# Performance work log

Hardware: AMD Instinct MI355X
Metric: run time of the kernel (lower is better)

## Reference

```python
import jax, jax.numpy as jnp
import numpy as np

B, T, C = 2, 2048, 1024
N_HEAD = 16
HEAD_DIM = C // N_HEAD


def setup_inputs() -> dict:
    key = jax.random.key(0)
    k1, k2, k3 = jax.random.split(key, 3)
    x = jax.random.normal(k1, (B, T, C), dtype=jnp.float32)
    w_attn = jax.random.normal(k2, (C, 3 * C), dtype=jnp.float32) * 0.02
    b_attn = jnp.zeros((3 * C,), dtype=jnp.float32)
    w_proj = jax.random.normal(k3, (C, C), dtype=jnp.float32) * 0.02
    b_proj = jnp.zeros((C,), dtype=jnp.float32)
    return {"x": x, "w_attn": w_attn, "b_attn": b_attn, "w_proj": w_proj, "b_proj": b_proj}


def reference(x, w_attn, b_attn, w_proj, b_proj):
    Bz, Tz, Cz = x.shape
    qkv = x @ w_attn + b_attn                       # [B, T, 3C]
    q, k, v = jnp.split(qkv, 3, axis=-1)
    # [B, H, T, D]
    q = q.reshape(Bz, Tz, N_HEAD, HEAD_DIM).transpose(0, 2, 1, 3)
    k = k.reshape(Bz, Tz, N_HEAD, HEAD_DIM).transpose(0, 2, 1, 3)
    v = v.reshape(Bz, Tz, N_HEAD, HEAD_DIM).transpose(0, 2, 1, 3)
    scale = 1.0 / np.sqrt(HEAD_DIM).astype(np.float32)
    att = jnp.einsum('bhqd,bhkd->bhqk', q, k) * scale  # [B, H, T, T]
    causal = jnp.tril(jnp.ones((Tz, Tz), dtype=bool))
    att = jnp.where(causal[None, None], att, -jnp.inf)
    att = jax.nn.softmax(att, axis=-1)
    y = jnp.einsum('bhqk,bhkd->bhqd', att, v)          # [B, H, T, D]
    y = y.transpose(0, 2, 1, 3).reshape(Bz, Tz, Cz)
    return y @ w_proj + b_proj
```

## Files before the change

### kernel.cpp

```cpp
#include <hip/hip_runtime.h>
#include <stdint.h>

#define T_SEQ 2048
#define NH 16
#define HD 64
#define M_DIM 4096
#define K_DIM 1024

typedef __attribute__((ext_vector_type(8))) short bf16x8;
typedef __attribute__((ext_vector_type(4))) short bf16x4;
typedef __attribute__((ext_vector_type(4))) float f32x4;
typedef __attribute__((ext_vector_type(4))) unsigned short u16x4;

__device__ __forceinline__ unsigned short f2bf(float f) {
  union { float f; uint32_t u; } x; x.f = f;
  uint32_t u = x.u;
  return (unsigned short)((u + 0x7fffu + ((u >> 16) & 1u)) >> 16);
}

__device__ __forceinline__ uint32_t cvtpk_bf16(float a, float b) {
  uint32_t r;
  asm("v_cvt_pk_bf16_f32 %0, %1, %2" : "=v"(r) : "v"(a), "v"(b));
  return r;
}

__device__ __forceinline__ f32x4 mfma16(bf16x4 a, bf16x4 b, f32x4 c) {
  asm("v_mfma_f32_16x16x16_bf16 %0, %1, %2, %0" : "+v"(c) : "v"(a), "v"(b));
  return c;
}

#define GLOAD16(g, l) __builtin_amdgcn_global_load_lds( \
    (const __attribute__((address_space(1))) unsigned int*)(g), \
    (__attribute__((address_space(3))) unsigned int*)(l), 16, 0, 0)

__device__ __forceinline__ void do_convert(const float* __restrict__ src,
                                           unsigned short* __restrict__ dst, int bid) {
  int idx = (bid * 256 + threadIdx.x) * 4;
  f32x4 v = *(const f32x4*)(src + idx);
  u16x4 o;
  #pragma unroll
  for (int i = 0; i < 4; ++i) o[i] = f2bf(v[i]);
  *(u16x4*)(dst + idx) = o;
}

__device__ __forceinline__ void do_transpose(const float* __restrict__ src,
                                             unsigned short* __restrict__ dst,
                                             int R, int Cn, int bx, int by,
                                             float (*tile)[65]) {
  const int r0 = by * 64, c0 = bx * 64;
  const int t = threadIdx.x;
  const int rr = t >> 4;
  const int c4 = (t & 15) * 4;
  #pragma unroll
  for (int p = 0; p < 4; ++p) {
    f32x4 v = *(const f32x4*)(src + (size_t)(r0 + p * 16 + rr) * Cn + c0 + c4);
    #pragma unroll
    for (int i = 0; i < 4; ++i) tile[p * 16 + rr][c4 + i] = v[i];
  }
  __syncthreads();
  #pragma unroll
  for (int p = 0; p < 4; ++p) {
    const int cl = p * 16 + rr;
    u16x4 o;
    #pragma unroll
    for (int i = 0; i < 4; ++i) o[i] = f2bf(tile[c4 + i][cl]);
    *(u16x4*)(dst + (size_t)(c0 + cl) * R + r0 + c4) = o;
  }
}

__global__ __launch_bounds__(256) void prep_kernel(
    const float* __restrict__ x, unsigned short* __restrict__ xb,
    const float* __restrict__ w_attn, unsigned short* __restrict__ wqkvT,
    const float* __restrict__ w_proj, unsigned short* __restrict__ wprojT) {
  __shared__ float tile[64][65];
  const int b = blockIdx.x;
  if (b < 4096) {
    do_convert(x, xb, b);
  } else if (b < 4096 + 768) {
    const int bid = b - 4096;
    do_transpose(w_attn, wqkvT, 1024, 3072, bid % 48, bid / 48, tile);
  } else {
    const int bid = b - 4864;
    do_transpose(w_proj, wprojT, 1024, 1024, bid % 16, bid / 16, tile);
  }
}

template <int MODE, int WM>
__global__ __launch_bounds__(WM * 128) void gemm2_kernel(
    const unsigned short* __restrict__ A,
    const unsigned short* __restrict__ Bt,
    const float* __restrict__ bias,
    unsigned short* __restrict__ qout,
    unsigned short* __restrict__ kout,
    unsigned short* __restrict__ vTout,
    float* __restrict__ fout) {
  constexpr int BM = WM * 64;
  constexpr int NT = WM * 128;
  constexpr int U_A = BM * 4;
  constexpr int NU = (U_A + 512) / NT;
  __shared__ __align__(16) unsigned short As[2][BM * 32];
  __shared__ __align__(16) unsigned short Bs[2][128 * 32];
  const int t = threadIdx.x;
  const int w = t >> 6, l = t & 63;
  const int wr = w >> 1, wc = w & 1;
  const int lr = l & 15, lg = l >> 4;
  const int br = blockIdx.y, bc = blockIdx.x;

  f32x4 acc[4][4];
  const f32x4 zf = {0.f, 0.f, 0.f, 0.f};
  #pragma unroll
  for (int i = 0; i < 4; ++i)
    #pragma unroll
    for (int j = 0; j < 4; ++j) acc[i][j] = zf;

  const unsigned short* Abase = A + (size_t)(br * BM) * K_DIM;
  const unsigned short* Bbase = Bt + (size_t)(bc * 128) * K_DIM;

  #define STAGE(k0, buf) do {                                                    \
    _Pragma("unroll")                                                            \
    for (int i = 0; i < NU; ++i) {                                               \
      const int u = i * NT + t;                                                  \
      if (u < U_A) {                                                             \
        GLOAD16(Abase + (size_t)(u >> 2) * K_DIM + (k0) + (u & 3) * 8,           \
                &As[buf][u * 8]);                                                \
      } else {                                                                   \
        const int v = u - U_A;                                                   \
        GLOAD16(Bbase + (size_t)(v >> 2) * K_DIM + (k0) + (v & 3) * 8,           \
                &Bs[buf][v * 8]);                                                \
      }                                                                          \
    }                                                                            \
  } while (0)

  #define COMPUTE(buf) do {                                                      \
    bf16x8 af[4], bfv[4];                                                        \
    _Pragma("unroll")                                                            \
    for (int f = 0; f < 4; ++f) {                                                \
      af[f]  = *(const bf16x8*)(&As[buf][(wr * 64 + f * 16 + lr) * 32 + lg * 8]);\
      bfv[f] = *(const bf16x8*)(&Bs[buf][(wc * 64 + f * 16 + lr) * 32 + lg * 8]);\
    }                                                                            \
    _Pragma("unroll")                                                            \
    for (int fr = 0; fr < 4; ++fr)                                               \
      _Pragma("unroll")                                                          \
      for (int fc = 0; fc < 4; ++fc)                                             \
        acc[fr][fc] = __builtin_amdgcn_mfma_f32_16x16x32_bf16(af[fr], bfv[fc],   \
                                                              acc[fr][fc], 0, 0, 0); \
  } while (0)

  STAGE(0, 0);
  __syncthreads();
  #pragma unroll 1
  for (int k0 = 0; k0 < K_DIM; k0 += 64) {
    if (k0 + 32 < K_DIM) STAGE(k0 + 32, 1);
    COMPUTE(0);
    __syncthreads();
    if (k0 + 64 < K_DIM) STAGE(k0 + 64, 0);
    COMPUTE(1);
    __syncthreads();
  }
  #undef STAGE
  #undef COMPUTE

  #pragma unroll
  for (int fr = 0; fr < 4; ++fr) {
    #pragma unroll
    for (int fc = 0; fc < 4; ++fc) {
      const int m0 = br * BM + wr * 64 + fr * 16 + lg * 4;
      const int n  = bc * 128 + wc * 64 + fc * 16 + lr;
      if (MODE == 0) {
        const int which = n >> 10, rem = n & 1023;
        const int h = rem >> 6, d = rem & 63;
        const int b = m0 >> 11, tt0 = m0 & 2047;
        const int bh = b * NH + h;
        if (which == 2) {
          u16x4 pack;
          #pragma unroll
          for (int r = 0; r < 4; ++r) pack[r] = f2bf(acc[fr][fc][r] + bias[n]);
          *(u16x4*)(vTout + ((size_t)bh * HD + d) * T_SEQ + tt0) = pack;
        } else {
          unsigned short* o = (which == 0) ? qout : kout;
          const float sc = (which == 0) ? 0.18033688011112042f : 1.0f;
          #pragma unroll
          for (int r = 0; r < 4; ++r)
            o[((size_t)bh * T_SEQ + tt0 + r) * HD + d] = f2bf((acc[fr][fc][r] + bias[n]) * sc);
        }
      } else {
        #pragma unroll
        for (int r = 0; r < 4; ++r)
          fout[(size_t)(m0 + r) * 1024 + n] = acc[fr][fc][r] + bias[n];
      }
    }
  }
}

__global__ __launch_bounds__(256, 4) void flash_attn_kernel(
    const unsigned short* __restrict__ qg,
    const unsigned short* __restrict__ kg,
    const unsigned short* __restrict__ vTg,
    unsigned short* __restrict__ yg) {
  __shared__ __align__(16) unsigned short Ks[2][64 * 64];
  __shared__ __align__(16) unsigned short Vs[2][64 * 64];

  const int t = threadIdx.x;
  const int w = t >> 6, l = t & 63;
  const int lr = l & 15, lg = l >> 4;
  const int i = blockIdx.x;
  const int bh = (i & 7) * 4 + ((i >> 3) & 3);
  const int qt = 31 - (i >> 5);
  const int nt = qt + 1;
  const int qw = qt * 64 + w * 16;
  const int qrow = qw + lr;
  const int swz = lr & 7;

  const int srow0 = t >> 3;
  const int sch = t & 7;

  const size_t kgb = (size_t)bh * T_SEQ * HD;
  const size_t vgb = (size_t)bh * HD * T_SEQ;
  const f32x4 zf = {0.f, 0.f, 0.f, 0.f};

  const size_t qoff = ((size_t)bh * T_SEQ + qw + lr) * HD + lg * 8;
  const bf16x8 qf0 = *(const bf16x8*)(qg + qoff);
  const bf16x8 qf1 = *(const bf16x8*)(qg + qoff + 32);

  f32x4 acc[4];
  #pragma unroll
  for (int k = 0; k < 4; ++k) acc[k] = zf;
  float m_run = 0.f;
  float l_part = 0.f;

  #pragma unroll
  for (int sh = 0; sh < 2; ++sh) {
    const int row = sh * 32 + srow0;
    const int sc = (sch ^ (row & 7)) * 8;
    GLOAD16(kg + kgb + (size_t)row * HD + sc, Ks[0] + row * 64 + sch * 8);
    GLOAD16(vTg + vgb + (size_t)row * T_SEQ + sc, Vs[0] + row * 64 + sch * 8);
  }
  __syncthreads();

  int cur = 0;
  #pragma unroll 1
  for (int it = 0; it < nt; ++it) {
    const int kv0 = it * 64;
    if (it + 1 < nt) {
      const int kvn = kv0 + 64;
      #pragma unroll
      for (int sh = 0; sh < 2; ++sh) {
        const int row = sh * 32 + srow0;
        const int sc = (sch ^ (row & 7)) * 8;
        GLOAD16(kg + kgb + (size_t)(kvn + row) * HD + sc, Ks[cur ^ 1] + row * 64 + sch * 8);
        GLOAD16(vTg + vgb + (size_t)row * T_SEQ + kvn + sc, Vs[cur ^ 1] + row * 64 + sch * 8);
      }
    }

    f32x4 s[4];
    __builtin_amdgcn_s_setprio(1);
    #pragma unroll
    for (int fc = 0; fc < 4; ++fc) {
      const unsigned short* kr = Ks[cur] + (fc * 16 + lr) * 64;
      const bf16x8 k0v = *(const bf16x8*)(kr + ((lg ^ swz) * 8));
      const bf16x8 k1v = *(const bf16x8*)(kr + (((lg + 4) ^ swz) * 8));
      f32x4 sv = zf;
      sv = __builtin_amdgcn_mfma_f32_16x16x32_bf16(k0v, qf0, sv, 0, 0, 0);
      sv = __builtin_amdgcn_mfma_f32_16x16x32_bf16(k1v, qf1, sv, 0, 0, 0);
      s[fc] = sv;
    }
    __builtin_amdgcn_s_setprio(0);

    if (it == nt - 1) {
      #pragma unroll
      for (int fc = 0; fc < 4; ++fc)
        #pragma unroll
        for (int r = 0; r < 4; ++r) {
          const int tkv = kv0 + fc * 16 + lg * 4 + r;
          if (tkv > qrow) s[fc][r] = -1e30f;
        }
    }

    float mt = s[0][0];
    #pragma unroll
    for (int fc = 0; fc < 4; ++fc)
      #pragma unroll
      for (int r = 0; r < 4; ++r) mt = fmaxf(mt, s[fc][r]);
    if (__any(mt > m_run + 8.f)) {
      float mrow = fmaxf(mt, __shfl_xor(mt, 16));
      mrow = fmaxf(mrow, __shfl_xor(mrow, 32));
      const float m_new = fmaxf(m_run, mrow);
      const float fac = __builtin_amdgcn_exp2f(m_run - m_new);
      l_part *= fac;
      float frs[4];
      #pragma unroll
      for (int r = 0; r < 4; ++r) frs[r] = __shfl(fac, lg * 4 + r);
      #pragma unroll
      for (int fd = 0; fd < 4; ++fd)
        #pragma unroll
        for (int r = 0; r < 4; ++r) acc[fd][r] *= frs[r];
      m_run = m_new;
    }

    union { uint32_t d[2]; bf16x4 v; } pkd[4];
    #pragma unroll
    for (int fc = 0; fc < 4; ++fc) {
      float e0 = __builtin_amdgcn_exp2f(s[fc][0] - m_run);
      float e1 = __builtin_amdgcn_exp2f(s[fc][1] - m_run);
      float e2 = __builtin_amdgcn_exp2f(s[fc][2] - m_run);
      float e3 = __builtin_amdgcn_exp2f(s[fc][3] - m_run);
      l_part += (e0 + e1) + (e2 + e3);
      pkd[fc].d[0] = cvtpk_bf16(e0, e1);
      pkd[fc].d[1] = cvtpk_bf16(e2, e3);
    }

    __builtin_amdgcn_s_setprio(1);
    #pragma unroll
    for (int fd = 0; fd < 4; ++fd) {
      const unsigned short* vr = Vs[cur] + (fd * 16 + lr) * 64;
      bf16x4 vf[4];
      #pragma unroll
      for (int fc = 0; fc < 4; ++fc) {
        const int ch = (fc * 2 + (lg >> 1)) ^ swz;
        vf[fc] = *(const bf16x4*)(vr + ch * 8 + (lg & 1) * 4);
      }
      f32x4 a = acc[fd];
      #pragma unroll
      for (int fc = 0; fc < 4; ++fc) a = mfma16(pkd[fc].v, vf[fc], a);
      acc[fd] = a;
    }
    __builtin_amdgcn_s_setprio(0);
    __syncthreads();
    cur ^= 1;
  }

  float lsum = l_part;
  lsum += __shfl_xor(lsum, 16);
  lsum += __shfl_xor(lsum, 32);

  const int b = bh >> 4, h = bh & 15;
  #pragma unroll
  for (int r = 0; r < 4; ++r) {
    const float lv = __shfl(lsum, lg * 4 + r);
    const float linv = 1.f / lv;
    const int tt = qw + lg * 4 + r;
    #pragma unroll
    for (int fd = 0; fd < 4; ++fd) {
      const int d = fd * 16 + lr;
      yg[(((size_t)b * T_SEQ + tt) * NH + h) * HD + d] = f2bf(acc[fd][r] * linv);
    }
  }
}

extern "C" void kernel_launch(void* const* d_in, const int* in_sizes, int n_in,
                              void* d_out, int out_size, void* d_ws, size_t ws_size,
                              hipStream_t stream) {
  (void)in_sizes; (void)n_in; (void)out_size; (void)ws_size;
  const float* x      = (const float*)d_in[0];
  const float* w_attn = (const float*)d_in[1];
  const float* b_attn = (const float*)d_in[2];
  const float* w_proj = (const float*)d_in[3];
  const float* b_proj = (const float*)d_in[4];
  float* out = (float*)d_out;

  char* ws = (char*)d_ws;
  unsigned short* xb     = (unsigned short*)(ws);
  unsigned short* wqkvT  = (unsigned short*)(ws + (8ull  << 20));
  unsigned short* wprojT = (unsigned short*)(ws + (14ull << 20));
  unsigned short* qb     = (unsigned short*)(ws + (16ull << 20));
  unsigned short* kb     = (unsigned short*)(ws + (24ull << 20));
  unsigned short* vT     = (unsigned short*)(ws + (32ull << 20));
  unsigned short* yb     = (unsigned short*)(ws + (40ull << 20));

  prep_kernel<<<5120, 256, 0, stream>>>(x, xb, w_attn, wqkvT, w_proj, wprojT);
  gemm2_kernel<0, 2><<<dim3(24, 32), 256, 0, stream>>>(xb, wqkvT, b_attn, qb, kb, vT, nullptr);
  flash_attn_kernel<<<1024, 256, 0, stream>>>(qb, kb, vT, yb);
  gemm2_kernel<1, 2><<<dim3(8, 32), 256, 0, stream>>>(yb, wprojT, b_proj, nullptr, nullptr, nullptr, out);
}
```

Before: 193.7 us.

## Use triple-buffered async GEMM pipeline with one barrier per k-step and XCD-aware block remap

Replaces the double-buffered GEMM loop, which had two barriers per iteration, with a three-stage LDS ring. Loads for k-step ks+2 are issued while ks is computed, and each step waits with a partial vmcnt followed by a single barrier. Workgroup IDs are also remapped so that consecutive tiles land on the same XCD, which should improve L2 reuse. The aim is to hide global-load latency better in both the QKV and output projections, at the cost of more LDS per block (48KB) and possibly lower occupancy.

```diff
diff --git a/kernel.cpp b/kernel.cpp
--- a/kernel.cpp
+++ b/kernel.cpp
@@ -85,8 +85,8 @@
   }
 }
 
-template <int MODE, int WM>
-__global__ __launch_bounds__(WM * 128) void gemm2_kernel(
+template <int MODE>
+__global__ __launch_bounds__(256, 3) void gemm3_kernel(
     const unsigned short* __restrict__ A,
     const unsigned short* __restrict__ Bt,
     const float* __restrict__ bias,
@@ -94,17 +94,17 @@
     unsigned short* __restrict__ kout,
     unsigned short* __restrict__ vTout,
     float* __restrict__ fout) {
-  constexpr int BM = WM * 64;
-  constexpr int NT = WM * 128;
-  constexpr int U_A = BM * 4;
-  constexpr int NU = (U_A + 512) / NT;
-  __shared__ __align__(16) unsigned short As[2][BM * 32];
-  __shared__ __align__(16) unsigned short Bs[2][128 * 32];
+  constexpr int NS = K_DIM / 32;
+  constexpr int NWG = (MODE == 0) ? 768 : 256;
+  constexpr int NBC = (MODE == 0) ? 24 : 8;
+  __shared__ __align__(16) unsigned short As[3][128 * 32];
+  __shared__ __align__(16) unsigned short Bs[3][128 * 32];
   const int t = threadIdx.x;
   const int w = t >> 6, l = t & 63;
   const int wr = w >> 1, wc = w & 1;
   const int lr = l & 15, lg = l >> 4;
-  const int br = blockIdx.y, bc = blockIdx.x;
+  const int wg = (blockIdx.x & 7) * (NWG >> 3) + (blockIdx.x >> 3);
+  const int bc = wg % NBC, br = wg / NBC;
 
   f32x4 acc[4][4];
   const f32x4 zf = {0.f, 0.f, 0.f, 0.f};
@@ -113,30 +113,29 @@
     #pragma unroll
     for (int j = 0; j < 4; ++j) acc[i][j] = zf;
 
-  const unsigned short* Abase = A + (size_t)(br * BM) * K_DIM;
+  const unsigned short* Abase = A + (size_t)(br * 128) * K_DIM;
   const unsigned short* Bbase = Bt + (size_t)(bc * 128) * K_DIM;
-
-  #define STAGE(k0, buf) do {                                                    \
-    _Pragma("unroll")                                                            \
-    for (int i = 0; i < NU; ++i) {                                               \
-      const int u = i * NT + t;                                                  \
-      if (u < U_A) {                                                             \
-        GLOAD16(Abase + (size_t)(u >> 2) * K_DIM + (k0) + (u & 3) * 8,           \
-                &As[buf][u * 8]);                                                \
-      } else {                                                                   \
-        const int v = u - U_A;                                                   \
-        GLOAD16(Bbase + (size_t)(v >> 2) * K_DIM + (k0) + (v & 3) * 8,           \
-                &Bs[buf][v * 8]);                                                \
-      }                                                                          \
-    }                                                                            \
+  const int uA0 = t, uA1 = t + 256;
+  const int uB0 = t, uB1 = t + 256;
+
+  #define STAGE(ks, buf) do {                                                   \
+    const int k0 = (ks) * 32;                                                   \
+    unsigned short* as = &As[0][0] + (buf) * (128 * 32);                        \
+    unsigned short* bs = &Bs[0][0] + (buf) * (128 * 32);                        \
+    GLOAD16(Abase + (size_t)(uA0 >> 2) * K_DIM + k0 + (uA0 & 3) * 8, as + uA0 * 8); \
+    GLOAD16(Abase + (size_t)(uA1 >> 2) * K_DIM + k0 + (uA1 & 3) * 8, as + uA1 * 8); \
+    GLOAD16(Bbase + (size_t)(uB0 >> 2) * K_DIM + k0 + (uB0 & 3) * 8, bs + uB0 * 8); \
+    GLOAD16(Bbase + (size_t)(uB1 >> 2) * K_DIM + k0 + (uB1 & 3) * 8, bs + uB1 * 8); \
   } while (0)
 
   #define COMPUTE(buf) do {                                                      \
+    const unsigned short* as = &As[0][0] + (buf) * (128 * 32);                   \
+    const unsigned short* bs = &Bs[0][0] + (buf) * (128 * 32);                   \
     bf16x8 af[4], bfv[4];                                                        \
     _Pragma("unroll")                                                            \
     for (int f = 0; f < 4; ++f) {                                                \
-      af[f]  = *(const bf16x8*)(&As[buf][(wr * 64 + f * 16 + lr) * 32 + lg * 8]);\
-      bfv[f] = *(const bf16x8*)(&Bs[buf][(wc * 64 + f * 16 + lr) * 32 + lg * 8]);\
+      af[f]  = *(const bf16x8*)(as + (wr * 64 + f * 16 + lr) * 32 + lg * 8);     \
+      bfv[f] = *(const bf16x8*)(bs + (wc * 64 + f * 16 + lr) * 32 + lg * 8);     \
     }                                                                            \
     _Pragma("unroll")                                                            \
     for (int fr = 0; fr < 4; ++fr)                                               \
@@ -147,15 +146,23 @@
   } while (0)
 
   STAGE(0, 0);
-  __syncthreads();
+  STAGE(1, 1);
+  int b_cur = 0;
   #pragma unroll 1
-  for (int k0 = 0; k0 < K_DIM; k0 += 64) {
-    if (k0 + 32 < K_DIM) STAGE(k0 + 32, 1);
-    COMPUTE(0);
-    __syncthreads();
-    if (k0 + 64 < K_DIM) STAGE(k0 + 64, 0);
-    COMPUTE(1);
-    __syncthreads();
+  for (int ks = 0; ks < NS; ++ks) {
+    if (ks == NS - 1) {
+      asm volatile("s_waitcnt vmcnt(0)" ::: "memory");
+    } else {
+      asm volatile("s_waitcnt vmcnt(4)" ::: "memory");
+    }
+    __builtin_amdgcn_sched_barrier(0);
+    __builtin_amdgcn_s_barrier();
+    if (ks + 2 < NS) {
+      const int b_stg = (b_cur == 0) ? 2 : b_cur - 1;
+      STAGE(ks + 2, b_stg);
+    }
+    COMPUTE(b_cur);
+    b_cur = (b_cur == 2) ? 0 : b_cur + 1;
   }
   #undef STAGE
   #undef COMPUTE
@@ -164,7 +171,7 @@
   for (int fr = 0; fr < 4; ++fr) {
     #pragma unroll
     for (int fc = 0; fc < 4; ++fc) {
-      const int m0 = br * BM + wr * 64 + fr * 16 + lg * 4;
+      const int m0 = br * 128 + wr * 64 + fr * 16 + lg * 4;
       const int n  = bc * 128 + wc * 64 + fc * 16 + lr;
       if (MODE == 0) {
         const int which = n >> 10, rem = n & 1023;
@@ -368,7 +375,7 @@
   unsigned short* yb     = (unsigned short*)(ws + (40ull << 20));
 
   prep_kernel<<<5120, 256, 0, stream>>>(x, xb, w_attn, wqkvT, w_proj, wprojT);
-  gemm2_kernel<0, 2><<<dim3(24, 32), 256, 0, stream>>>(xb, wqkvT, b_attn, qb, kb, vT, nullptr);
+  gemm3_kernel<0><<<768, 256, 0, stream>>>(xb, wqkvT, b_attn, qb, kb, vT, nullptr);
   flash_attn_kernel<<<1024, 256, 0, stream>>>(qb, kb, vT, yb);
-  gemm2_kernel<1, 2><<<dim3(8, 32), 256, 0, stream>>>(yb, wprojT, b_proj, nullptr, nullptr, nullptr, out);
-}
+  gemm3_kernel<1><<<256, 256, 0, stream>>>(yb, wprojT, b_proj, nullptr, nullptr, nullptr, out);
+}
```

After: 179.9 us. 1.08x faster.
